# Performance work log

Measured on AMD Instinct MI355X. Metric: run time of the kernel, lower is better.

Reference implementation:

```python
import jax, jax.numpy as jnp
import numpy as np

FEATURE_DIM = 6272
UNITS = 32
B, L = 8, 256

def setup_inputs() -> dict:
    key = jax.random.key(0)
    k1, k2, k3, k4, k5 = jax.random.split(key, 5)
    return {
        "inputs": jax.random.normal(k1, (B, L, FEATURE_DIM), dtype=jnp.float32),
        "Wt": jax.random.normal(k2, (FEATURE_DIM, UNITS), dtype=jnp.float32) * 0.02,
        "bh": jax.random.normal(k3, (UNITS,), dtype=jnp.float32),
        "Wa": jax.random.normal(k4, (UNITS, 1), dtype=jnp.float32) * 0.02,
        "ba": jax.random.normal(k5, (1,), dtype=jnp.float32),
    }

def reference(inputs, Wt, bh, Wa, ba):
    # q == k: both projected through Wt (original code reuses Wt for both)
    p = jnp.einsum('blf,fu->blu', inputs, Wt)            # [B, L, U]
    # additive (Bahdanau-style) pairwise combine: [B, L, L, U]
    beta = jnp.tanh(p[:, :, None, :] + p[:, None, :, :] + bh)
    alpha = jnp.einsum('bqku,uo->bqk', beta, Wa) + ba[0]  # [B, L, L]
    alpha = jax.nn.sigmoid(alpha)
    a = jax.nn.softmax(alpha, axis=-1)                    # softmax over keys
    c_r = jnp.einsum('bqk,bkf->bqf', a, inputs)           # [B, L, F]
    return c_r
```

## Files before the change

kernel.cpp:

```cpp
#include <hip/hip_runtime.h>
#include <hip/hip_bf16.h>
#include <math.h>

#define FDIM 6272
#define LQ   256
#define BN   8
#define UDIM 32
#define BL   (BN*LQ)
#define FSPL 448
#define NSPL 14
#define WTS2 456

typedef short  short8 __attribute__((ext_vector_type(8)));
typedef float  f32x4  __attribute__((ext_vector_type(4)));

static __device__ __forceinline__ ushort f2bf(float f) {
    __hip_bfloat16 h = __float2bfloat16(f);
    return *(ushort*)&h;
}
static __device__ __forceinline__ float fexp2(float x) {
    float r;
    asm volatile("v_exp_f32 %0, %1 \n s_nop 1" : "=v"(r) : "v"(x));
    return r;
}
static __device__ __forceinline__ float frcp(float x) {
    float r;
    asm volatile("v_rcp_f32 %0, %1 \n s_nop 1" : "=v"(r) : "v"(x));
    return r;
}
static __device__ __forceinline__ float tanh_fast(float v) {
    return 1.f - 2.f * frcp(1.f + fexp2(v * 2.88539008177793f));
}

__global__ __launch_bounds__(256)
void k1_mfma(const float* __restrict__ x, const float* __restrict__ Wt,
             float* __restrict__ pbp, ushort* __restrict__ xb16) {
    __shared__ ushort wtt_s[UDIM * WTS2];

    const int t  = threadIdx.x;
    const int f0 = blockIdx.y * FSPL;

    {
        const int fl0 = t >> 3;
        const int u4  = (t & 7) * 4;
        #pragma unroll
        for (int s = 0; s < NSPL; ++s) {
            const int fl = s * 32 + fl0;
            const float4 w4 = *(const float4*)(Wt + (size_t)(f0 + fl) * UDIM + u4);
            wtt_s[(u4 + 0) * WTS2 + fl] = f2bf(w4.x);
            wtt_s[(u4 + 1) * WTS2 + fl] = f2bf(w4.y);
            wtt_s[(u4 + 2) * WTS2 + fl] = f2bf(w4.z);
            wtt_s[(u4 + 3) * WTS2 + fl] = f2bf(w4.w);
        }
    }
    __syncthreads();

    const int wv   = t >> 6, lane = t & 63;
    const int n16  = lane & 15, quad = lane >> 4;
    const int row0 = blockIdx.x * 64 + 16 * wv;

    const float*  xr  = x + (size_t)(row0 + n16) * FDIM + f0 + quad * 8;
    const ushort* wr0 = wtt_s + (     n16) * WTS2 + quad * 8;
    const ushort* wr1 = wtt_s + (16 + n16) * WTS2 + quad * 8;
    ushort*       xw  = xb16 + (size_t)(row0 + n16) * FDIM + f0 + quad * 8;

    f32x4 acc0 = (f32x4){0.f, 0.f, 0.f, 0.f};
    f32x4 acc1 = (f32x4){0.f, 0.f, 0.f, 0.f};

    #pragma unroll 7
    for (int c = 0; c < NSPL; ++c) {
        const float4 a0 = *(const float4*)(xr + c * 32);
        const float4 a1 = *(const float4*)(xr + c * 32 + 4);
        short8 af;
        af[0] = (short)f2bf(a0.x); af[1] = (short)f2bf(a0.y);
        af[2] = (short)f2bf(a0.z); af[3] = (short)f2bf(a0.w);
        af[4] = (short)f2bf(a1.x); af[5] = (short)f2bf(a1.y);
        af[6] = (short)f2bf(a1.z); af[7] = (short)f2bf(a1.w);
        *(short8*)(xw + c * 32) = af;
        const short8 b0 = *(const short8*)(wr0 + c * 32);
        const short8 b1 = *(const short8*)(wr1 + c * 32);
        acc0 = __builtin_amdgcn_mfma_f32_16x16x32_bf16(af, b0, acc0, 0, 0, 0);
        acc1 = __builtin_amdgcn_mfma_f32_16x16x32_bf16(af, b1, acc1, 0, 0, 0);
    }

    float* pb = pbp + (size_t)blockIdx.y * BL * UDIM;
    #pragma unroll
    for (int r = 0; r < 4; ++r) {
        pb[(size_t)(row0 + quad * 4 + r) * UDIM +      n16] = acc0[r];
        pb[(size_t)(row0 + quad * 4 + r) * UDIM + 16 + n16] = acc1[r];
    }
}

__global__ __launch_bounds__(256)
void k2_attn(const float* __restrict__ pbp, const float* __restrict__ bh,
             const float* __restrict__ Wa, const float* __restrict__ ba,
             ushort* __restrict__ ab) {
    const int blk = blockIdx.x;
    const int b   = blk >> 6, qt = blk & 63;
    const int k   = threadIdx.x;

    __shared__ float pk_s[LQ * 33];
    __shared__ float pq_s[4][UDIM];
    __shared__ float wa_s[UDIM];
    __shared__ float red[4][4];

    if (k < UDIM) wa_s[k] = Wa[k];
    const float* pbb = pbp + (size_t)b * LQ * UDIM;
    #pragma unroll
    for (int i = 0; i < 8; ++i) {
        const int e = 4 * k + 1024 * i;
        float4 v = *(const float4*)(pbb + e);
        #pragma unroll
        for (int y = 1; y < NSPL; ++y) {
            const float4 p = *(const float4*)(pbb + (size_t)y * BL * UDIM + e);
            v.x += p.x; v.y += p.y; v.z += p.z; v.w += p.w;
        }
        float* d = &pk_s[(e >> 5) * 33 + (e & 31)];
        d[0] = v.x; d[1] = v.y; d[2] = v.z; d[3] = v.w;
    }
    __syncthreads();
    if (k < 4 * UDIM) {
        const int j = k >> 5, u = k & 31;
        pq_s[j][u] = pk_s[(qt * 4 + j) * 33 + u] + bh[u];
    }
    __syncthreads();

    const float* pk = &pk_s[k * 33];
    float pkr[UDIM];
    #pragma unroll
    for (int u = 0; u < UDIM; ++u) pkr[u] = pk[u];

    const float ba0 = ba[0];
    float e4[4];
    #pragma unroll
    for (int j = 0; j < 4; ++j) {
        float s = 0.f;
        #pragma unroll
        for (int u = 0; u < UDIM; ++u)
            s = fmaf(tanh_fast(pq_s[j][u] + pkr[u]), wa_s[u], s);

        const float alpha = frcp(1.f + fexp2(-(s + ba0) * 1.44269504088896f));
        const float e = fexp2(alpha * 1.44269504088896f);
        e4[j] = e;

        float v = e;
        #pragma unroll
        for (int m = 1; m < 64; m <<= 1) v += __shfl_xor(v, m, 64);
        if ((k & 63) == 0) red[j][k >> 6] = v;
    }
    __syncthreads();
    #pragma unroll
    for (int j = 0; j < 4; ++j) {
        const float tot = red[j][0] + red[j][1] + red[j][2] + red[j][3];
        ab[((size_t)b * LQ + qt * 4 + j) * LQ + k] = f2bf(e4[j] * frcp(tot));
    }
}

__global__ __launch_bounds__(256)
void k3_fused(const ushort* __restrict__ xb16, const ushort* __restrict__ ab,
              float* __restrict__ out) {
    __shared__ ushort Bs[2][64 * 72];

    const int t    = threadIdx.x;
    const int f0   = blockIdx.x * 64;
    const int b    = blockIdx.y;
    const int wv   = t >> 6;
    const int lane = t & 63;
    const int n16  = lane & 15;
    const int quad = lane >> 4;
    const int g    = t >> 4;
    const int kp   = t & 15;

    const ushort* xb  = xb16 + (size_t)b * LQ * FDIM + f0 + 4 * g;
    const ushort* abb = ab   + (size_t)b * LQ * LQ;

    f32x4 acc[4][4];
    #pragma unroll
    for (int mf = 0; mf < 4; ++mf)
        #pragma unroll
        for (int nf = 0; nf < 4; ++nf)
            acc[mf][nf] = (f32x4){0.f, 0.f, 0.f, 0.f};

    uint2 r0, r1, r2, r3;
#define LDX(kc) do {                                                      \
        r0 = *(const uint2*)(xb + (size_t)((kc) + 2 * kp     ) * FDIM);   \
        r1 = *(const uint2*)(xb + (size_t)((kc) + 2 * kp +  1) * FDIM);   \
        r2 = *(const uint2*)(xb + (size_t)((kc) + 2 * kp + 32) * FDIM);   \
        r3 = *(const uint2*)(xb + (size_t)((kc) + 2 * kp + 33) * FDIM);   \
    } while (0)
#define STX(bufi) do {                                                    \
        unsigned* bw = (unsigned*)(Bs[bufi]);                             \
        bw[(4 * g + 0) * 36 + kp]      = (r0.x & 0xffffu) | (r1.x << 16); \
        bw[(4 * g + 1) * 36 + kp]      = (r0.x >> 16) | (r1.x & 0xffff0000u); \
        bw[(4 * g + 2) * 36 + kp]      = (r0.y & 0xffffu) | (r1.y << 16); \
        bw[(4 * g + 3) * 36 + kp]      = (r0.y >> 16) | (r1.y & 0xffff0000u); \
        bw[(4 * g + 0) * 36 + kp + 16] = (r2.x & 0xffffu) | (r3.x << 16); \
        bw[(4 * g + 1) * 36 + kp + 16] = (r2.x >> 16) | (r3.x & 0xffff0000u); \
        bw[(4 * g + 2) * 36 + kp + 16] = (r2.y & 0xffffu) | (r3.y << 16); \
        bw[(4 * g + 3) * 36 + kp + 16] = (r2.y >> 16) | (r3.y & 0xffff0000u); \
    } while (0)

    LDX(0);
    STX(0);

    for (int c = 0; c < 4; ++c) {
        if (c < 3) LDX((c + 1) * 64);
        short8 af[4][2];
        #pragma unroll
        for (int mf = 0; mf < 4; ++mf)
            #pragma unroll
            for (int h = 0; h < 2; ++h)
                af[mf][h] = *(const short8*)(abb
                    + (size_t)(64 * wv + 16 * mf + n16) * LQ
                    + c * 64 + h * 32 + quad * 8);
        __syncthreads();
        const ushort* bsc = Bs[c & 1];
        #pragma unroll
        for (int h = 0; h < 2; ++h)
            #pragma unroll
            for (int nf = 0; nf < 4; ++nf) {
                const short8 bf = *(const short8*)(bsc + (16 * nf + n16) * 72
                                                   + h * 32 + quad * 8);
                #pragma unroll
                for (int mf = 0; mf < 4; ++mf)
                    acc[mf][nf] = __builtin_amdgcn_mfma_f32_16x16x32_bf16(
                        af[mf][h], bf, acc[mf][nf], 0, 0, 0);
            }
        if (c < 3) STX((c + 1) & 1);
    }
#undef LDX
#undef STX

    float* ob = out + ((size_t)b * LQ + 64 * wv + quad * 4) * FDIM + f0 + n16;
    #pragma unroll
    for (int mf = 0; mf < 4; ++mf)
        #pragma unroll
        for (int nf = 0; nf < 4; ++nf)
            #pragma unroll
            for (int r = 0; r < 4; ++r)
                ob[(size_t)(16 * mf + r) * FDIM + 16 * nf] = acc[mf][nf][r];
}

extern "C" void kernel_launch(void* const* d_in, const int* in_sizes, int n_in,
                              void* d_out, int out_size, void* d_ws, size_t ws_size,
                              hipStream_t stream) {
    const float* x  = (const float*)d_in[0];
    const float* Wt = (const float*)d_in[1];
    const float* bh = (const float*)d_in[2];
    const float* Wa = (const float*)d_in[3];
    const float* ba = (const float*)d_in[4];
    float* out = (float*)d_out;

    float*  pbp  = (float*)d_ws;
    ushort* ab   = (ushort*)((char*)d_ws + 4194304);
    ushort* xb16 = (ushort*)((char*)d_ws + 4194304 + 1048576);

    k1_mfma<<<dim3(32, NSPL), 256, 0, stream>>>(x, Wt, pbp, xb16);
    k2_attn<<<512, 256, 0, stream>>>(pbp, bh, Wa, ba, ab);
    k3_fused<<<dim3(98, 8), 256, 0, stream>>>(xb16, ab, out);
}
```

Before: 156.7 us.

## Drop bf16 copy of inputs; convert fp32 on the fly in final GEMM

The first kernel no longer writes a bf16 copy of the inputs. The final attention-times-inputs kernel now reads the fp32 inputs directly and converts them to bf16 while staging into shared memory. This removes a 26MB write and trades a 26MB bf16 read for a 51MB fp32 read that may partly hit cache. Separately, the attention kernel now handles 8 query rows per block instead of 4, with two accumulators to shorten the dependency chain, which halves the grid and the redundant reloading of the key projections.

After: 152.3 us. 2.8% less time.

```diff
diff --git a/kernel.cpp b/kernel.cpp
--- a/kernel.cpp
+++ b/kernel.cpp
@@ -34,7 +34,7 @@
 
 __global__ __launch_bounds__(256)
 void k1_mfma(const float* __restrict__ x, const float* __restrict__ Wt,
-             float* __restrict__ pbp, ushort* __restrict__ xb16) {
+             float* __restrict__ pbp) {
     __shared__ ushort wtt_s[UDIM * WTS2];
 
     const int t  = threadIdx.x;
@@ -62,7 +62,6 @@
     const float*  xr  = x + (size_t)(row0 + n16) * FDIM + f0 + quad * 8;
     const ushort* wr0 = wtt_s + (     n16) * WTS2 + quad * 8;
     const ushort* wr1 = wtt_s + (16 + n16) * WTS2 + quad * 8;
-    ushort*       xw  = xb16 + (size_t)(row0 + n16) * FDIM + f0 + quad * 8;
 
     f32x4 acc0 = (f32x4){0.f, 0.f, 0.f, 0.f};
     f32x4 acc1 = (f32x4){0.f, 0.f, 0.f, 0.f};
@@ -76,7 +75,6 @@
         af[2] = (short)f2bf(a0.z); af[3] = (short)f2bf(a0.w);
         af[4] = (short)f2bf(a1.x); af[5] = (short)f2bf(a1.y);
         af[6] = (short)f2bf(a1.z); af[7] = (short)f2bf(a1.w);
-        *(short8*)(xw + c * 32) = af;
         const short8 b0 = *(const short8*)(wr0 + c * 32);
         const short8 b1 = *(const short8*)(wr1 + c * 32);
         acc0 = __builtin_amdgcn_mfma_f32_16x16x32_bf16(af, b0, acc0, 0, 0, 0);
@@ -96,13 +94,13 @@
              const float* __restrict__ Wa, const float* __restrict__ ba,
              ushort* __restrict__ ab) {
     const int blk = blockIdx.x;
-    const int b   = blk >> 6, qt = blk & 63;
+    const int b   = blk >> 5, qt = blk & 31;
     const int k   = threadIdx.x;
 
     __shared__ float pk_s[LQ * 33];
-    __shared__ float pq_s[4][UDIM];
+    __shared__ float pq_s[8][UDIM];
     __shared__ float wa_s[UDIM];
-    __shared__ float red[4][4];
+    __shared__ float red[8][4];
 
     if (k < UDIM) wa_s[k] = Wa[k];
     const float* pbb = pbp + (size_t)b * LQ * UDIM;
@@ -119,9 +117,9 @@
         d[0] = v.x; d[1] = v.y; d[2] = v.z; d[3] = v.w;
     }
     __syncthreads();
-    if (k < 4 * UDIM) {
+    {
         const int j = k >> 5, u = k & 31;
-        pq_s[j][u] = pk_s[(qt * 4 + j) * 33 + u] + bh[u];
+        pq_s[j][u] = pk_s[(qt * 8 + j) * 33 + u] + bh[u];
     }
     __syncthreads();
 
@@ -131,17 +129,20 @@
     for (int u = 0; u < UDIM; ++u) pkr[u] = pk[u];
 
     const float ba0 = ba[0];
-    float e4[4];
-    #pragma unroll
-    for (int j = 0; j < 4; ++j) {
-        float s = 0.f;
-        #pragma unroll
-        for (int u = 0; u < UDIM; ++u)
-            s = fmaf(tanh_fast(pq_s[j][u] + pkr[u]), wa_s[u], s);
+    float e8[8];
+    #pragma unroll
+    for (int j = 0; j < 8; ++j) {
+        float s0 = 0.f, s1 = 0.f;
+        #pragma unroll
+        for (int u = 0; u < UDIM; u += 2) {
+            s0 = fmaf(tanh_fast(pq_s[j][u    ] + pkr[u    ]), wa_s[u    ], s0);
+            s1 = fmaf(tanh_fast(pq_s[j][u + 1] + pkr[u + 1]), wa_s[u + 1], s1);
+        }
+        const float s = s0 + s1;
 
         const float alpha = frcp(1.f + fexp2(-(s + ba0) * 1.44269504088896f));
         const float e = fexp2(alpha * 1.44269504088896f);
-        e4[j] = e;
+        e8[j] = e;
 
         float v = e;
         #pragma unroll
@@ -150,14 +151,14 @@
     }
     __syncthreads();
     #pragma unroll
-    for (int j = 0; j < 4; ++j) {
+    for (int j = 0; j < 8; ++j) {
         const float tot = red[j][0] + red[j][1] + red[j][2] + red[j][3];
-        ab[((size_t)b * LQ + qt * 4 + j) * LQ + k] = f2bf(e4[j] * frcp(tot));
+        ab[((size_t)b * LQ + qt * 8 + j) * LQ + k] = f2bf(e8[j] * frcp(tot));
     }
 }
 
 __global__ __launch_bounds__(256)
-void k3_fused(const ushort* __restrict__ xb16, const ushort* __restrict__ ab,
+void k3_fused(const float* __restrict__ x, const ushort* __restrict__ ab,
               float* __restrict__ out) {
     __shared__ ushort Bs[2][64 * 72];
 
@@ -171,8 +172,8 @@
     const int g    = t >> 4;
     const int kp   = t & 15;
 
-    const ushort* xb  = xb16 + (size_t)b * LQ * FDIM + f0 + 4 * g;
-    const ushort* abb = ab   + (size_t)b * LQ * LQ;
+    const float*  xb  = x  + (size_t)b * LQ * FDIM + f0 + 4 * g;
+    const ushort* abb = ab + (size_t)b * LQ * LQ;
 
     f32x4 acc[4][4];
     #pragma unroll
@@ -181,23 +182,23 @@
         for (int nf = 0; nf < 4; ++nf)
             acc[mf][nf] = (f32x4){0.f, 0.f, 0.f, 0.f};
 
-    uint2 r0, r1, r2, r3;
+    float4 r0, r1, r2, r3;
 #define LDX(kc) do {                                                      \
-        r0 = *(const uint2*)(xb + (size_t)((kc) + 2 * kp     ) * FDIM);   \
-        r1 = *(const uint2*)(xb + (size_t)((kc) + 2 * kp +  1) * FDIM);   \
-        r2 = *(const uint2*)(xb + (size_t)((kc) + 2 * kp + 32) * FDIM);   \
-        r3 = *(const uint2*)(xb + (size_t)((kc) + 2 * kp + 33) * FDIM);   \
+        r0 = *(const float4*)(xb + (size_t)((kc) + 2 * kp     ) * FDIM);  \
+        r1 = *(const float4*)(xb + (size_t)((kc) + 2 * kp +  1) * FDIM);  \
+        r2 = *(const float4*)(xb + (size_t)((kc) + 2 * kp + 32) * FDIM);  \
+        r3 = *(const float4*)(xb + (size_t)((kc) + 2 * kp + 33) * FDIM);  \
     } while (0)
-#define STX(bufi) do {                                                    \
-        unsigned* bw = (unsigned*)(Bs[bufi]);                             \
-        bw[(4 * g + 0) * 36 + kp]      = (r0.x & 0xffffu) | (r1.x << 16); \
-        bw[(4 * g + 1) * 36 + kp]      = (r0.x >> 16) | (r1.x & 0xffff0000u); \
-        bw[(4 * g + 2) * 36 + kp]      = (r0.y & 0xffffu) | (r1.y << 16); \
-        bw[(4 * g + 3) * 36 + kp]      = (r0.y >> 16) | (r1.y & 0xffff0000u); \
-        bw[(4 * g + 0) * 36 + kp + 16] = (r2.x & 0xffffu) | (r3.x << 16); \
-        bw[(4 * g + 1) * 36 + kp + 16] = (r2.x >> 16) | (r3.x & 0xffff0000u); \
-        bw[(4 * g + 2) * 36 + kp + 16] = (r2.y & 0xffffu) | (r3.y << 16); \
-        bw[(4 * g + 3) * 36 + kp + 16] = (r2.y >> 16) | (r3.y & 0xffff0000u); \
+#define STX(bufi) do {                                                        \
+        unsigned* bw = (unsigned*)(Bs[bufi]);                                 \
+        bw[(4 * g + 0) * 36 + kp]      = (unsigned)f2bf(r0.x) | ((unsigned)f2bf(r1.x) << 16); \
+        bw[(4 * g + 1) * 36 + kp]      = (unsigned)f2bf(r0.y) | ((unsigned)f2bf(r1.y) << 16); \
+        bw[(4 * g + 2) * 36 + kp]      = (unsigned)f2bf(r0.z) | ((unsigned)f2bf(r1.z) << 16); \
+        bw[(4 * g + 3) * 36 + kp]      = (unsigned)f2bf(r0.w) | ((unsigned)f2bf(r1.w) << 16); \
+        bw[(4 * g + 0) * 36 + kp + 16] = (unsigned)f2bf(r2.x) | ((unsigned)f2bf(r3.x) << 16); \
+        bw[(4 * g + 1) * 36 + kp + 16] = (unsigned)f2bf(r2.y) | ((unsigned)f2bf(r3.y) << 16); \
+        bw[(4 * g + 2) * 36 + kp + 16] = (unsigned)f2bf(r2.z) | ((unsigned)f2bf(r3.z) << 16); \
+        bw[(4 * g + 3) * 36 + kp + 16] = (unsigned)f2bf(r2.w) | ((unsigned)f2bf(r3.w) << 16); \
     } while (0)
 
     LDX(0);
@@ -251,11 +252,10 @@
     const float* ba = (const float*)d_in[4];
     float* out = (float*)d_out;
 
-    float*  pbp  = (float*)d_ws;
-    ushort* ab   = (ushort*)((char*)d_ws + 4194304);
-    ushort* xb16 = (ushort*)((char*)d_ws + 4194304 + 1048576);
-
-    k1_mfma<<<dim3(32, NSPL), 256, 0, stream>>>(x, Wt, pbp, xb16);
-    k2_attn<<<512, 256, 0, stream>>>(pbp, bh, Wa, ba, ab);
-    k3_fused<<<dim3(98, 8), 256, 0, stream>>>(xb16, ab, out);
-}
+    float*  pbp = (float*)d_ws;
+    ushort* ab  = (ushort*)((char*)d_ws + 4194304);
+
+    k1_mfma<<<dim3(32, NSPL), 256, 0, stream>>>(x, Wt, pbp);
+    k2_attn<<<256, 256, 0, stream>>>(pbp, bh, Wa, ba, ab);
+    k3_fused<<<dim3(98, 8), 256, 0, stream>>>(x, ab, out);
+}
```
